# Kernel tuning notes

Measured on AMD Instinct MI355X. Metric: run time of the kernel, lower is better.

Reference implementation:

```python
import jax, jax.numpy as jnp
import numpy as np

N_HEADS = 16
N_EMBD = 1024

def setup_inputs() -> dict:
    key = jax.random.key(0)
    k1, k2, k3, k4, k5 = jax.random.split(key, 5)
    B, T, C = 4, 2048, N_EMBD
    x = jax.random.normal(k1, (B, T, C), dtype=jnp.float32)
    # Linear weights stored as [in, out] (equivalent math to torch's x @ W.T + b)
    W_attn = jax.random.normal(k2, (C, 3 * C), dtype=jnp.float32) * 0.02
    b_attn = jax.random.normal(k3, (3 * C,), dtype=jnp.float32) * 0.02
    W_proj = jax.random.normal(k4, (C, C), dtype=jnp.float32) * 0.02
    b_proj = jax.random.normal(k5, (C,), dtype=jnp.float32) * 0.02
    return {"x": x, "W_attn": W_attn, "b_attn": b_attn, "W_proj": W_proj, "b_proj": b_proj}

def reference(x, W_attn, b_attn, W_proj, b_proj):
    B, T, C = x.shape
    H = N_HEADS
    D = C // H
    scale = 1.0 / jnp.sqrt(jnp.asarray(D, dtype=x.dtype))
    # fused QKV projection
    qkv = x @ W_attn + b_attn                      # [B, T, 3C]
    q, k, v = jnp.split(qkv, 3, axis=-1)           # each [B, T, C]
    q = q.reshape(B, T, H, D)
    k = k.reshape(B, T, H, D)
    v = v.reshape(B, T, H, D)
    # non-causal SDPA
    scores = jnp.einsum('bqhd,bkhd->bhqk', q, k) * scale  # [B, H, T, T]
    attn = jax.nn.softmax(scores, axis=-1)
    y = jnp.einsum('bhqk,bkhd->bqhd', attn, v)     # [B, T, H, D]
    y = y.reshape(B, T, C)
    return y @ W_proj + b_proj
```

## Files before the change

### kernel.cpp

```cpp
#include <hip/hip_runtime.h>

typedef short s16x8 __attribute__((ext_vector_type(8)));
typedef float f32x4 __attribute__((ext_vector_type(4)));

__device__ __forceinline__ unsigned short f2bf(float f) {
  unsigned u = __float_as_uint(f);
  u += 0x7fffu + ((u >> 16) & 1u);
  return (unsigned short)(u >> 16);
}
__device__ __forceinline__ float bf2f(unsigned short h) {
  return __uint_as_float(((unsigned)h) << 16);
}


__global__ __launch_bounds__(256) void cvt_x_bf16(const float* __restrict__ in,
                                                  unsigned short* __restrict__ out) {
  int i = (blockIdx.x * 256 + threadIdx.x) * 4;
  float4 v = *(const float4*)(in + i);
  ushort4 o;
  o.x = f2bf(v.x); o.y = f2bf(v.y); o.z = f2bf(v.z); o.w = f2bf(v.w);
  *(ushort4*)(out + i) = o;
}

__global__ __launch_bounds__(256) void transpose_w(const float* __restrict__ W,
                                                   unsigned short* __restrict__ Wt,
                                                   int R, int C) {
  __shared__ float tile[32][33];
  int c0 = blockIdx.x * 32, r0 = blockIdx.y * 32;
  int x = threadIdx.x, ty = threadIdx.y;
  for (int yy = ty; yy < 32; yy += 8)
    tile[yy][x] = W[(size_t)(r0 + yy) * C + c0 + x];
  __syncthreads();
  for (int yy = ty; yy < 32; yy += 8)
    Wt[(size_t)(c0 + yy) * R + r0 + x] = f2bf(tile[x][yy]);
}

__global__ __launch_bounds__(256) void transpose_v(const unsigned short* __restrict__ qkv,
                                                   unsigned short* __restrict__ vt) {
  __shared__ unsigned short TT[32][72];
  const int bh = blockIdx.y;
  const int t0 = blockIdx.x * 32;
  const int b = bh >> 4, h = bh & 15;
  const int t = threadIdx.x;
  {
    int row = t >> 3, c8 = (t & 7) * 8;
    const unsigned short* src =
        qkv + (size_t)(b * 2048 + t0 + row) * 3072 + 2048 + h * 64 + c8;
    *(uint4*)&TT[row][c8] = *(const uint4*)src;
  }
  __syncthreads();
  {
    int drow = t >> 2, tc8 = (t & 3) * 8;
    uint4 val;
    unsigned short* vp = (unsigned short*)&val;
    for (int j = 0; j < 8; j++) vp[j] = TT[tc8 + j][drow];
    *(uint4*)(vt + (size_t)(bh * 64 + drow) * 2048 + t0 + tc8) = val;
  }
}


template <bool OUT_BF16>
__global__ __launch_bounds__(256) void gemm_bt(const unsigned short* __restrict__ A,
                                               const unsigned short* __restrict__ Bt,
                                               const float* __restrict__ bias,
                                               void* __restrict__ Cout,
                                               int M, int N, int K) {
  __shared__ __align__(16) unsigned short As[128][40];
  __shared__ __align__(16) unsigned short Bs[128][40];

  const int tid  = threadIdx.x;
  const int lane = tid & 63;
  const int w    = tid >> 6;
  const int lr   = lane & 15;
  const int quad = lane >> 4;
  const int wm   = (w >> 1) * 64;
  const int wn   = (w & 1) * 64;
  const int m0   = blockIdx.y * 128;
  const int n0   = blockIdx.x * 128;

  f32x4 acc[4][4];
  for (int i = 0; i < 4; i++)
    for (int j = 0; j < 4; j++)
      acc[i][j] = f32x4{0.f, 0.f, 0.f, 0.f};

  const int srow = tid >> 2;
  const int scb  = (tid & 3) * 8;
  const unsigned short* Ap = A  + (size_t)(m0 + srow) * K + scb;
  const unsigned short* Bp = Bt + (size_t)(n0 + srow) * K + scb;

  for (int kk = 0; kk < K; kk += 32) {
    __syncthreads();
    *(uint4*)&As[srow][scb]      = *(const uint4*)(Ap + kk);
    *(uint4*)&As[srow + 64][scb] = *(const uint4*)(Ap + (size_t)64 * K + kk);
    *(uint4*)&Bs[srow][scb]      = *(const uint4*)(Bp + kk);
    *(uint4*)&Bs[srow + 64][scb] = *(const uint4*)(Bp + (size_t)64 * K + kk);
    __syncthreads();

    s16x8 af[4], bf[4];
    for (int i = 0; i < 4; i++) af[i] = *(const s16x8*)&As[wm + i * 16 + lr][quad * 8];
    for (int j = 0; j < 4; j++) bf[j] = *(const s16x8*)&Bs[wn + j * 16 + lr][quad * 8];
    for (int i = 0; i < 4; i++)
      for (int j = 0; j < 4; j++)
        acc[i][j] = __builtin_amdgcn_mfma_f32_16x16x32_bf16(af[i], bf[j], acc[i][j], 0, 0, 0);
  }

  for (int j = 0; j < 4; j++) {
    int col = n0 + wn + j * 16 + lr;
    float bc = bias[col];
    for (int i = 0; i < 4; i++) {
      int rowb = m0 + wm + i * 16 + quad * 4;
      for (int r = 0; r < 4; r++) {
        float v = acc[i][j][r] + bc;
        if (OUT_BF16)
          ((unsigned short*)Cout)[(size_t)(rowb + r) * N + col] = f2bf(v);
        else
          ((float*)Cout)[(size_t)(rowb + r) * N + col] = v;
      }
    }
  }
}


__global__ __launch_bounds__(256, 4) void attn_flash(const unsigned short* __restrict__ qkv,
                                                     const unsigned short* __restrict__ vt,
                                                     unsigned short* __restrict__ y) {
  const int T = 2048, C3 = 3072;
  const int qt = blockIdx.x & 15;
  const int bh = blockIdx.x >> 4;
  const int b  = bh >> 4;
  const int h  = bh & 15;
  const int q0 = qt * 128;

  const int tid  = threadIdx.x;
  const int lane = tid & 63;
  const int w    = tid >> 6;
  const int lr   = lane & 15;
  const int quad = lane >> 4;

  __shared__ __align__(16) unsigned short Ks[64][72];
  __shared__ __align__(16) unsigned short Vs[64][72];
  __shared__ __align__(16) unsigned short Ps[4][32][72];

  s16x8 qf[2][2];
  const float QSC = 0.18033688f;
  for (int i = 0; i < 2; i++)
    for (int c = 0; c < 2; c++) {
      const unsigned short* qp =
          qkv + (size_t)(b * T + q0 + w * 32 + i * 16 + lr) * C3 + h * 64 + c * 32 + quad * 8;
      s16x8 t = *(const s16x8*)qp;
      s16x8 o;
      for (int j = 0; j < 8; j++)
        o[j] = (short)f2bf(bf2f((unsigned short)t[j]) * QSC);
      qf[i][c] = o;
    }

  f32x4 O[2][4];
  for (int i = 0; i < 2; i++)
    for (int dt = 0; dt < 4; dt++) O[i][dt] = f32x4{0.f, 0.f, 0.f, 0.f};
  float l[2][4] = {{0.f, 0.f, 0.f, 0.f}, {0.f, 0.f, 0.f, 0.f}};

  const int srow = tid >> 3;
  const int sc8  = (tid & 7) * 8;
  const unsigned short* kbase = qkv + (size_t)(b * T) * C3 + 1024 + (size_t)h * 64;
  const unsigned short* vbase = vt + (size_t)(bh * 64) * 2048;

  for (int kt = 0; kt < 32; kt++) {
    const int k0 = kt * 64;
    __syncthreads();
    *(uint4*)&Ks[srow][sc8]      = *(const uint4*)(kbase + (size_t)(k0 + srow) * C3 + sc8);
    *(uint4*)&Ks[srow + 32][sc8] = *(const uint4*)(kbase + (size_t)(k0 + srow + 32) * C3 + sc8);
    *(uint4*)&Vs[srow][sc8]      = *(const uint4*)(vbase + (size_t)srow * 2048 + k0 + sc8);
    *(uint4*)&Vs[srow + 32][sc8] = *(const uint4*)(vbase + (size_t)(srow + 32) * 2048 + k0 + sc8);
    __syncthreads();

    f32x4 S[2][4];
    for (int i = 0; i < 2; i++)
      for (int j = 0; j < 4; j++) S[i][j] = f32x4{0.f, 0.f, 0.f, 0.f};
    for (int c = 0; c < 2; c++) {
      s16x8 kf[4];
      for (int j = 0; j < 4; j++)
        kf[j] = *(const s16x8*)&Ks[j * 16 + lr][c * 32 + quad * 8];
      for (int i = 0; i < 2; i++)
        for (int j = 0; j < 4; j++)
          S[i][j] = __builtin_amdgcn_mfma_f32_16x16x32_bf16(qf[i][c], kf[j], S[i][j], 0, 0, 0);
    }

    for (int i = 0; i < 2; i++)
      for (int r = 0; r < 4; r++) {
        float p0 = __builtin_amdgcn_exp2f(S[i][0][r]);
        float p1 = __builtin_amdgcn_exp2f(S[i][1][r]);
        float p2 = __builtin_amdgcn_exp2f(S[i][2][r]);
        float p3 = __builtin_amdgcn_exp2f(S[i][3][r]);
        l[i][r] += (p0 + p1) + (p2 + p3);
        int row = i * 16 + quad * 4 + r;
        Ps[w][row][lr]      = f2bf(p0);
        Ps[w][row][16 + lr] = f2bf(p1);
        Ps[w][row][32 + lr] = f2bf(p2);
        Ps[w][row][48 + lr] = f2bf(p3);
      }

    for (int c = 0; c < 2; c++) {
      s16x8 pf0 = *(const s16x8*)&Ps[w][lr][c * 32 + quad * 8];
      s16x8 pf1 = *(const s16x8*)&Ps[w][16 + lr][c * 32 + quad * 8];
      for (int dt = 0; dt < 4; dt++) {
        s16x8 vf = *(const s16x8*)&Vs[dt * 16 + lr][c * 32 + quad * 8];
        O[0][dt] = __builtin_amdgcn_mfma_f32_16x16x32_bf16(pf0, vf, O[0][dt], 0, 0, 0);
        O[1][dt] = __builtin_amdgcn_mfma_f32_16x16x32_bf16(pf1, vf, O[1][dt], 0, 0, 0);
      }
    }
  }

  for (int i = 0; i < 2; i++)
    for (int r = 0; r < 4; r++) {
      float s = l[i][r];
      s += __shfl_xor(s, 1, 16);
      s += __shfl_xor(s, 2, 16);
      s += __shfl_xor(s, 4, 16);
      s += __shfl_xor(s, 8, 16);
      l[i][r] = 1.f / s;
    }
  for (int i = 0; i < 2; i++)
    for (int dt = 0; dt < 4; dt++) {
      int col = h * 64 + dt * 16 + lr;
      for (int r = 0; r < 4; r++) {
        int row = b * T + q0 + w * 32 + i * 16 + quad * 4 + r;
        y[(size_t)row * 1024 + col] = f2bf(O[i][dt][r] * l[i][r]);
      }
    }
}


extern "C" void kernel_launch(void* const* d_in, const int* in_sizes, int n_in,
                              void* d_out, int out_size, void* d_ws, size_t ws_size,
                              hipStream_t stream) {
  const float* x  = (const float*)d_in[0];
  const float* Wa = (const float*)d_in[1];
  const float* ba = (const float*)d_in[2];
  const float* Wp = (const float*)d_in[3];
  const float* bp = (const float*)d_in[4];
  float* out = (float*)d_out;

  char* ws = (char*)d_ws;
  unsigned short* xb  = (unsigned short*)ws;
  unsigned short* Wat = (unsigned short*)(ws + 16777216);
  unsigned short* Wpt = (unsigned short*)(ws + 23068672);
  unsigned short* qkv = (unsigned short*)(ws + 25165824);
  unsigned short* vtr = (unsigned short*)(ws + 75497472);

  cvt_x_bf16<<<8192, 256, 0, stream>>>(x, xb);
  transpose_w<<<dim3(96, 32), dim3(32, 8), 0, stream>>>(Wa, Wat, 1024, 3072);
  transpose_w<<<dim3(32, 32), dim3(32, 8), 0, stream>>>(Wp, Wpt, 1024, 1024);

  gemm_bt<true><<<dim3(24, 64), 256, 0, stream>>>(xb, Wat, ba, qkv, 8192, 3072, 1024);

  transpose_v<<<dim3(64, 64), 256, 0, stream>>>(qkv, vtr);

  attn_flash<<<1024, 256, 0, stream>>>(qkv, vtr, xb);

  gemm_bt<false><<<dim3(8, 64), 256, 0, stream>>>(xb, Wpt, bp, out, 8192, 1024, 1024);
}
```

Baseline: 313.9 us.

## Use direct global-to-LDS loads in GEMM and enlarge attention query tile

The GEMM now stages A and B tiles with global_load_lds straight into unpadded shared memory, skipping the register round trip. The attention kernel doubles the query tile per block to 256 rows (64 per wave), so each K/V tile loaded into LDS is reused across twice as many queries. The block count halves and the launch bound drops to 2 blocks per CU. P values are now packed in pairs with DPP lane swaps and written as 32-bit stores. Risks include higher register pressure, lower occupancy, fewer blocks to fill the CUs, and LDS bank conflicts from the unpadded GEMM tiles.

```diff
diff --git a/kernel.cpp b/kernel.cpp
--- a/kernel.cpp
+++ b/kernel.cpp
@@ -11,6 +11,11 @@
 __device__ __forceinline__ float bf2f(unsigned short h) {
   return __uint_as_float(((unsigned)h) << 16);
 }
+
+#define GLOAD_LDS16(g, l)                                          \
+  __builtin_amdgcn_global_load_lds(                                \
+      (const __attribute__((address_space(1))) void*)(g),          \
+      (__attribute__((address_space(3))) void*)(l), 16, 0, 0)
 
 
 __global__ __launch_bounds__(256) void cvt_x_bf16(const float* __restrict__ in,
@@ -65,8 +70,8 @@
                                                const float* __restrict__ bias,
                                                void* __restrict__ Cout,
                                                int M, int N, int K) {
-  __shared__ __align__(16) unsigned short As[128][40];
-  __shared__ __align__(16) unsigned short Bs[128][40];
+  __shared__ __align__(16) unsigned short As[128 * 32];
+  __shared__ __align__(16) unsigned short Bs[128 * 32];
 
   const int tid  = threadIdx.x;
   const int lane = tid & 63;
@@ -87,18 +92,22 @@
   const int scb  = (tid & 3) * 8;
   const unsigned short* Ap = A  + (size_t)(m0 + srow) * K + scb;
   const unsigned short* Bp = Bt + (size_t)(n0 + srow) * K + scb;
+  unsigned short* lA0 = As + w * 512;
+  unsigned short* lA1 = As + 2048 + w * 512;
+  unsigned short* lB0 = Bs + w * 512;
+  unsigned short* lB1 = Bs + 2048 + w * 512;
 
   for (int kk = 0; kk < K; kk += 32) {
     __syncthreads();
-    *(uint4*)&As[srow][scb]      = *(const uint4*)(Ap + kk);
-    *(uint4*)&As[srow + 64][scb] = *(const uint4*)(Ap + (size_t)64 * K + kk);
-    *(uint4*)&Bs[srow][scb]      = *(const uint4*)(Bp + kk);
-    *(uint4*)&Bs[srow + 64][scb] = *(const uint4*)(Bp + (size_t)64 * K + kk);
+    GLOAD_LDS16(Ap + kk, lA0);
+    GLOAD_LDS16(Ap + (size_t)64 * K + kk, lA1);
+    GLOAD_LDS16(Bp + kk, lB0);
+    GLOAD_LDS16(Bp + (size_t)64 * K + kk, lB1);
     __syncthreads();
 
     s16x8 af[4], bf[4];
-    for (int i = 0; i < 4; i++) af[i] = *(const s16x8*)&As[wm + i * 16 + lr][quad * 8];
-    for (int j = 0; j < 4; j++) bf[j] = *(const s16x8*)&Bs[wn + j * 16 + lr][quad * 8];
+    for (int i = 0; i < 4; i++) af[i] = *(const s16x8*)&As[(wm + i * 16 + lr) * 32 + quad * 8];
+    for (int j = 0; j < 4; j++) bf[j] = *(const s16x8*)&Bs[(wn + j * 16 + lr) * 32 + quad * 8];
     for (int i = 0; i < 4; i++)
       for (int j = 0; j < 4; j++)
         acc[i][j] = __builtin_amdgcn_mfma_f32_16x16x32_bf16(af[i], bf[j], acc[i][j], 0, 0, 0);
@@ -121,15 +130,15 @@
 }
 
 
-__global__ __launch_bounds__(256, 4) void attn_flash(const unsigned short* __restrict__ qkv,
+__global__ __launch_bounds__(256, 2) void attn_flash(const unsigned short* __restrict__ qkv,
                                                      const unsigned short* __restrict__ vt,
                                                      unsigned short* __restrict__ y) {
   const int T = 2048, C3 = 3072;
-  const int qt = blockIdx.x & 15;
-  const int bh = blockIdx.x >> 4;
+  const int qt = blockIdx.x & 7;
+  const int bh = blockIdx.x >> 3;
   const int b  = bh >> 4;
   const int h  = bh & 15;
-  const int q0 = qt * 128;
+  const int q0 = qt * 256;
 
   const int tid  = threadIdx.x;
   const int lane = tid & 63;
@@ -139,14 +148,14 @@
 
   __shared__ __align__(16) unsigned short Ks[64][72];
   __shared__ __align__(16) unsigned short Vs[64][72];
-  __shared__ __align__(16) unsigned short Ps[4][32][72];
-
-  s16x8 qf[2][2];
+  __shared__ __align__(16) unsigned short Ps[4][64][72];
+
+  s16x8 qf[4][2];
   const float QSC = 0.18033688f;
-  for (int i = 0; i < 2; i++)
+  for (int i = 0; i < 4; i++)
     for (int c = 0; c < 2; c++) {
       const unsigned short* qp =
-          qkv + (size_t)(b * T + q0 + w * 32 + i * 16 + lr) * C3 + h * 64 + c * 32 + quad * 8;
+          qkv + (size_t)(b * T + q0 + w * 64 + i * 16 + lr) * C3 + h * 64 + c * 32 + quad * 8;
       s16x8 t = *(const s16x8*)qp;
       s16x8 o;
       for (int j = 0; j < 8; j++)
@@ -154,16 +163,21 @@
       qf[i][c] = o;
     }
 
-  f32x4 O[2][4];
-  for (int i = 0; i < 2; i++)
+  f32x4 O[4][4];
+  for (int i = 0; i < 4; i++)
     for (int dt = 0; dt < 4; dt++) O[i][dt] = f32x4{0.f, 0.f, 0.f, 0.f};
-  float l[2][4] = {{0.f, 0.f, 0.f, 0.f}, {0.f, 0.f, 0.f, 0.f}};
+  float l[4][4];
+  for (int i = 0; i < 4; i++)
+    for (int r = 0; r < 4; r++) l[i][r] = 0.f;
 
   const int srow = tid >> 3;
   const int sc8  = (tid & 7) * 8;
   const unsigned short* kbase = qkv + (size_t)(b * T) * C3 + 1024 + (size_t)h * 64;
   const unsigned short* vbase = vt + (size_t)(bh * 64) * 2048;
 
+  const int odd   = lr & 1;
+  const int colp0 = lr & ~1;
+
   for (int kt = 0; kt < 32; kt++) {
     const int k0 = kt * 64;
     __syncthreads();
@@ -173,44 +187,48 @@
     *(uint4*)&Vs[srow + 32][sc8] = *(const uint4*)(vbase + (size_t)(srow + 32) * 2048 + k0 + sc8);
     __syncthreads();
 
-    f32x4 S[2][4];
-    for (int i = 0; i < 2; i++)
-      for (int j = 0; j < 4; j++) S[i][j] = f32x4{0.f, 0.f, 0.f, 0.f};
+    s16x8 kf[2][4];
+    for (int c = 0; c < 2; c++)
+      for (int j = 0; j < 4; j++)
+        kf[c][j] = *(const s16x8*)&Ks[j * 16 + lr][c * 32 + quad * 8];
+
+    for (int i = 0; i < 4; i++) {
+      f32x4 S[4];
+      for (int j = 0; j < 4; j++) S[j] = f32x4{0.f, 0.f, 0.f, 0.f};
+      for (int c = 0; c < 2; c++)
+        for (int j = 0; j < 4; j++)
+          S[j] = __builtin_amdgcn_mfma_f32_16x16x32_bf16(qf[i][c], kf[c][j], S[j], 0, 0, 0);
+
+      for (int j = 0; j < 4; j++) {
+        unsigned pk[4];
+        for (int r = 0; r < 4; r++) {
+          float p = __builtin_amdgcn_exp2f(S[j][r]);
+          l[i][r] += p;
+          unsigned u = (unsigned)f2bf(p);
+          unsigned nb = (unsigned)__builtin_amdgcn_mov_dpp((int)u, 0xB1, 0xF, 0xF, true);
+          pk[r] = odd ? (nb | (u << 16)) : (u | (nb << 16));
+        }
+        int rb  = odd * 2;
+        int row = i * 16 + quad * 4 + rb;
+        int cp  = j * 16 + colp0;
+        *(unsigned*)&Ps[w][row][cp]     = pk[rb];
+        *(unsigned*)&Ps[w][row + 1][cp] = pk[rb + 1];
+      }
+    }
+
     for (int c = 0; c < 2; c++) {
-      s16x8 kf[4];
-      for (int j = 0; j < 4; j++)
-        kf[j] = *(const s16x8*)&Ks[j * 16 + lr][c * 32 + quad * 8];
-      for (int i = 0; i < 2; i++)
-        for (int j = 0; j < 4; j++)
-          S[i][j] = __builtin_amdgcn_mfma_f32_16x16x32_bf16(qf[i][c], kf[j], S[i][j], 0, 0, 0);
-    }
-
-    for (int i = 0; i < 2; i++)
-      for (int r = 0; r < 4; r++) {
-        float p0 = __builtin_amdgcn_exp2f(S[i][0][r]);
-        float p1 = __builtin_amdgcn_exp2f(S[i][1][r]);
-        float p2 = __builtin_amdgcn_exp2f(S[i][2][r]);
-        float p3 = __builtin_amdgcn_exp2f(S[i][3][r]);
-        l[i][r] += (p0 + p1) + (p2 + p3);
-        int row = i * 16 + quad * 4 + r;
-        Ps[w][row][lr]      = f2bf(p0);
-        Ps[w][row][16 + lr] = f2bf(p1);
-        Ps[w][row][32 + lr] = f2bf(p2);
-        Ps[w][row][48 + lr] = f2bf(p3);
-      }
-
-    for (int c = 0; c < 2; c++) {
-      s16x8 pf0 = *(const s16x8*)&Ps[w][lr][c * 32 + quad * 8];
-      s16x8 pf1 = *(const s16x8*)&Ps[w][16 + lr][c * 32 + quad * 8];
-      for (int dt = 0; dt < 4; dt++) {
-        s16x8 vf = *(const s16x8*)&Vs[dt * 16 + lr][c * 32 + quad * 8];
-        O[0][dt] = __builtin_amdgcn_mfma_f32_16x16x32_bf16(pf0, vf, O[0][dt], 0, 0, 0);
-        O[1][dt] = __builtin_amdgcn_mfma_f32_16x16x32_bf16(pf1, vf, O[1][dt], 0, 0, 0);
-      }
-    }
-  }
-
-  for (int i = 0; i < 2; i++)
+      s16x8 vf[4];
+      for (int dt = 0; dt < 4; dt++)
+        vf[dt] = *(const s16x8*)&Vs[dt * 16 + lr][c * 32 + quad * 8];
+      for (int i = 0; i < 4; i++) {
+        s16x8 pf = *(const s16x8*)&Ps[w][i * 16 + lr][c * 32 + quad * 8];
+        for (int dt = 0; dt < 4; dt++)
+          O[i][dt] = __builtin_amdgcn_mfma_f32_16x16x32_bf16(pf, vf[dt], O[i][dt], 0, 0, 0);
+      }
+    }
+  }
+
+  for (int i = 0; i < 4; i++)
     for (int r = 0; r < 4; r++) {
       float s = l[i][r];
       s += __shfl_xor(s, 1, 16);
@@ -219,11 +237,11 @@
       s += __shfl_xor(s, 8, 16);
       l[i][r] = 1.f / s;
     }
-  for (int i = 0; i < 2; i++)
+  for (int i = 0; i < 4; i++)
     for (int dt = 0; dt < 4; dt++) {
       int col = h * 64 + dt * 16 + lr;
       for (int r = 0; r < 4; r++) {
-        int row = b * T + q0 + w * 32 + i * 16 + quad * 4 + r;
+        int row = b * T + q0 + w * 64 + i * 16 + quad * 4 + r;
         y[(size_t)row * 1024 + col] = f2bf(O[i][dt][r] * l[i][r]);
       }
     }
@@ -255,7 +273,7 @@
 
   transpose_v<<<dim3(64, 64), 256, 0, stream>>>(qkv, vtr);
 
-  attn_flash<<<1024, 256, 0, stream>>>(qkv, vtr, xb);
+  attn_flash<<<512, 256, 0, stream>>>(qkv, vtr, xb);
 
   gemm_bt<false><<<dim3(8, 64), 256, 0, stream>>>(xb, Wpt, bp, out, 8192, 1024, 1024);
 }
```

After: 351.7 us. +12.0%, slower.
